# Optimization experiments

Hardware: AMD Instinct MI355X
Metric: run time of the kernel (lower is better)

## Reference

```python
import jax, jax.numpy as jnp
import numpy as np
from jax import lax

STRIDE = (1, 1)
PADDING = ((1, 1), (1, 1))
DILATION = (1, 1)
GROUPS = 1


def setup_inputs() -> dict:
    key = jax.random.key(0)
    k1, k2, k3, k4, k5 = jax.random.split(key, 5)
    # quantized int8-ish activations/weights stored as float (as in the torch module)
    x = jax.random.randint(k1, (32, 128, 56, 56), -128, 128).astype(jnp.float32)
    weight_int = jax.random.randint(k2, (256, 128, 3, 3), -128, 128).astype(jnp.float32)
    bias_int = jax.random.randint(k3, (256,), -1024, 1024).astype(jnp.float32)
    A = jax.random.randint(k4, (256,), 1, 32768)  # per-channel requant multiplier
    N = jax.random.randint(k5, (256,), 16, 25)    # per-channel shift
    return {
        "x": x,
        "weight_int": weight_int,
        "bias_int": bias_int,
        "A": A,
        "N": N,
        "out_min": 0,
        "out_max": 255,
    }


def reference(x, weight_int, bias_int, A, N, out_min, out_max):
    # emulate torch's x.int().float() truncation casts
    xq = jnp.trunc(x)
    wq = jnp.trunc(weight_int)
    bq = jnp.trunc(bias_int)
    out = lax.conv_general_dilated(
        xq, wq,
        window_strides=STRIDE,
        padding=PADDING,
        rhs_dilation=DILATION,
        feature_group_count=GROUPS,
        dimension_numbers=("NCHW", "OIHW", "NCHW"),
    )
    out = jnp.round(out + bq[None, :, None, None])
    # out *= A ; out >>= N  (torch float rshift == divide by 2**N)
    Af = A.astype(jnp.float32)[None, :, None, None]
    Nf = N.astype(jnp.float32)[None, :, None, None]
    out = out * Af / jnp.exp2(Nf)
    if out_min >= 0:
        out = jnp.clip(jnp.round(out), float(out_min), float(out_max))
    return out
```

## Files before the change

### kernel.cpp

```cpp
#include <hip/hip_runtime.h>
#include <stdint.h>

typedef int   v4i __attribute__((ext_vector_type(4)));
typedef float v4f __attribute__((ext_vector_type(4)));

#define XT_H_STRIDE (66*128)
#define XT_N_STRIDE (58*66*128)
#define XT_BYTES    (32*58*66*128)
#define WQ_BYTES    (256*1152)

__device__ __forceinline__ void gload16(const void* g, void* l) {
  __builtin_amdgcn_global_load_lds(
      (const __attribute__((address_space(1))) void*)g,
      (__attribute__((address_space(3))) void*)l, 16, 0, 0);
}

__global__ __launch_bounds__(256) void xform_x(const float* __restrict__ x,
                                               char* __restrict__ xt) {
  __shared__ int LB[56 * 33];
  int bid = blockIdx.x;
  int n  = bid / 58;
  int hp = bid - n * 58;
  int t  = threadIdx.x;
  int srch = hp - 1;
  bool rowok = (srch >= 0) && (srch < 56);
  char* dstrow = xt + (size_t)n * XT_N_STRIDE + (size_t)hp * XT_H_STRIDE;

  if (rowok) {
    const float* rb = x + ((size_t)(n * 128) * 56 + srch) * 56;
#pragma unroll
    for (int u0 = 0; u0 < 2; ++u0) {
      int u  = t + u0 * 256;
      int wb = u & 15;
      int cb = u >> 4;
      int w0 = wb * 4, ci0 = cb * 4;
      if (w0 < 56) {
        int dw[4] = {0, 0, 0, 0};
#pragma unroll
        for (int i = 0; i < 4; ++i) {
          v4f f = *(const v4f*)(rb + (size_t)(ci0 + i) * 3136 + w0);
#pragma unroll
          for (int j = 0; j < 4; ++j)
            dw[j] |= (((int)f[j]) & 255) << (8 * i);
        }
#pragma unroll
        for (int j = 0; j < 4; ++j)
          LB[(w0 + j) * 33 + cb] = dw[j];
      }
    }
    __syncthreads();
    for (int c = t; c < 528; c += 256) {
      int wp  = c >> 3;
      int cio = c & 7;
      int srw = wp - 1;
      v4i v = {0, 0, 0, 0};
      if (srw >= 0 && srw < 56) {
#pragma unroll
        for (int k = 0; k < 4; ++k) v[k] = LB[srw * 33 + cio * 4 + k];
      }
      *(v4i*)(dstrow + c * 16) = v;
    }
  } else {
    v4i z = {0, 0, 0, 0};
    for (int c = t; c < 528; c += 256) *(v4i*)(dstrow + c * 16) = z;
  }
}

__global__ __launch_bounds__(256) void xform_w(const float* __restrict__ wsrc,
                                               const int* __restrict__ Aq,
                                               const int* __restrict__ Nq,
                                               char* __restrict__ wq2,
                                               float* __restrict__ scale) {
  int idx = blockIdx.x * 256 + threadIdx.x;
  int co = idx / 1152;
  int k  = idx - co * 1152;
  int g  = k >> 7;
  int ci = k & 127;
  int kh = g / 3;
  int kw = g - 3 * kh;
  float f = wsrc[(size_t)(co * 128 + ci) * 9 + kh * 3 + kw];
  wq2[((k >> 6) * 256 + co) * 64 + (k & 63)] = (signed char)(int)f;
  if (idx < 256) {
    scale[idx] = (float)Aq[idx] * exp2f(-(float)Nq[idx]);
  }
}

__global__ __launch_bounds__(256, 4) void qconv_gemm(
    const char* __restrict__ xt, const char* __restrict__ wq2,
    const float* __restrict__ bias, const float* __restrict__ scale,
    const int* __restrict__ pmin, const int* __restrict__ pmax,
    float* __restrict__ out) {
  __shared__ __align__(16) char Bp[4 * 8448];

  int bid = blockIdx.x;
  int xcd = bid & 7;
  int q   = bid >> 3;
  int mt  = q & 1;
  int nt  = xcd * 112 + (q >> 1);
  int n   = nt / 28;
  int ht  = nt - n * 28;
  int h0  = ht * 2;
  int m0  = mt * 128;

  int t  = threadIdx.x;
  int wv = t >> 6;
  int ln = t & 63;
  int quad = ln >> 4;
  int l16  = ln & 15;
  int wm = wv & 1, wn = wv >> 1;

  const char* xb = xt + (size_t)n * XT_N_STRIDE + (size_t)h0 * XT_H_STRIDE;

  for (int it = 0; it < 9; ++it) {
    int s = t + it * 256;
    if (s < 2112) {
      int row = s / 528;
      int rr  = s - row * 528;
      int w   = rr >> 3;
      int cq  = rr & 7;
      gload16(xb + row * XT_H_STRIDE + w * 128 + ((cq ^ (w & 7)) << 4),
              Bp + it * 4096 + wv * 1024);
    }
  }
  asm volatile("s_waitcnt vmcnt(0)" ::: "memory");
  asm volatile("s_barrier" ::: "memory");

  v4i acc[4][4];
#pragma unroll
  for (int i = 0; i < 4; ++i)
#pragma unroll
    for (int j = 0; j < 4; ++j) {
      v4i z = {0, 0, 0, 0};
      acc[i][j] = z;
    }

  const char* abase = wq2 + (size_t)(m0 + wm * 64 + l16) * 64 + quad * 16;

  for (int kt = 0; kt < 18; ++kt) {
    int p  = kt & 1;
    int g  = kt >> 1;
    int kh = g / 3;
    int kw = g - 3 * kh;

    v4i a[4], b[4];
    const char* akt = abase + ((size_t)kt << 14);
#pragma unroll
    for (int i = 0; i < 4; ++i)
      a[i] = *(const v4i*)(akt + i * 1024);

    int bswz = (((p << 2) + quad) ^ ((l16 + kw) & 7)) << 4;
    const char* bbase = Bp + (wn + kh) * XT_H_STRIDE + (l16 + kw) * 128 + bswz;
#pragma unroll
    for (int j = 0; j < 4; ++j)
      b[j] = *(const v4i*)(bbase + j * 2048);

#pragma unroll
    for (int i = 0; i < 4; ++i)
#pragma unroll
      for (int j = 0; j < 4; ++j)
        acc[i][j] = __builtin_amdgcn_mfma_i32_16x16x64_i8(a[i], b[j], acc[i][j], 0, 0, 0);
  }

  float mn = (float)pmin[0];
  float mx = (float)pmax[0];
#pragma unroll
  for (int i = 0; i < 4; ++i) {
    int co_b = m0 + wm * 64 + i * 16 + quad * 4;
#pragma unroll
    for (int r = 0; r < 4; ++r) {
      int co = co_b + r;
      float bs = bias[co];
      float sc = scale[co];
#pragma unroll
      for (int j = 0; j < 4; ++j) {
        int sl = wn * 64 + j * 16 + l16;
        int w  = sl & 63;
        int dh = sl >> 6;
        if (w < 56) {
          float f = (float)acc[i][j][r] + bs;
          f = rintf(f * sc);
          f = fminf(fmaxf(f, mn), mx);
          out[(((size_t)n * 256 + co) * 56 + (h0 + dh)) * 56 + w] = f;
        }
      }
    }
  }
}

extern "C" void kernel_launch(void* const* d_in, const int* in_sizes, int n_in,
                              void* d_out, int out_size, void* d_ws, size_t ws_size,
                              hipStream_t stream) {
  const float* x  = (const float*)d_in[0];
  const float* w  = (const float*)d_in[1];
  const float* b  = (const float*)d_in[2];
  const int*   Aq = (const int*)d_in[3];
  const int*   Nq = (const int*)d_in[4];
  const int*   mn = (const int*)d_in[5];
  const int*   mx = (const int*)d_in[6];
  float* out = (float*)d_out;

  char*  xt    = (char*)d_ws;
  char*  wq2   = xt + XT_BYTES;
  float* scale = (float*)(wq2 + WQ_BYTES);

  hipLaunchKernelGGL(xform_x, dim3(32 * 58), dim3(256), 0, stream, x, xt);
  hipLaunchKernelGGL(xform_w, dim3(1152), dim3(256), 0, stream, w, Aq, Nq, wq2, scale);
  hipLaunchKernelGGL(qconv_gemm, dim3(1792), dim3(256), 0, stream,
                     xt, wq2, b, scale, mn, mx, out);
}
```

Measured before the change: 194.3 us.

## Prefetch weight fragments three k-steps ahead with per-wave staggered k order

Keeps a three-deep register ring of A (weight) fragments, issuing their global loads before the LDS fill and three iterations ahead inside the fully unrolled k loop, so MFMAs no longer wait on global loads. Each wave starts its k sequence at a different offset to spread weight-load and LDS bank traffic. Output stores become nontemporal, and the launch-bounds occupancy hint drops from 4 to 3 blocks per CU to make room for the extra registers. The cost is higher register pressure and lower occupancy.

Measured after the change: 210.8 us. +8.5%, slower.

```diff
diff --git a/kernel.cpp b/kernel.cpp
--- a/kernel.cpp
+++ b/kernel.cpp
@@ -85,7 +85,7 @@
   }
 }
 
-__global__ __launch_bounds__(256, 4) void qconv_gemm(
+__global__ __launch_bounds__(256, 3) void qconv_gemm(
     const char* __restrict__ xt, const char* __restrict__ wq2,
     const float* __restrict__ bias, const float* __restrict__ scale,
     const int* __restrict__ pmin, const int* __restrict__ pmax,
@@ -111,6 +111,20 @@
 
   const char* xb = xt + (size_t)n * XT_N_STRIDE + (size_t)h0 * XT_H_STRIDE;
 
+  const char* abase = wq2 + (size_t)(m0 + wm * 64 + l16) * 64 + quad * 16;
+
+  int c5 = wv * 5;
+
+  v4i areg[3][4];
+#pragma unroll
+  for (int d = 0; d < 3; ++d) {
+    int kt = d + c5; if (kt >= 18) kt -= 18;
+    const char* akt = abase + ((size_t)kt << 14);
+#pragma unroll
+    for (int i = 0; i < 4; ++i)
+      areg[d][i] = *(const v4i*)(akt + i * 1024);
+  }
+
   for (int it = 0; it < 9; ++it) {
     int s = t + it * 256;
     if (s < 2112) {
@@ -134,22 +148,17 @@
       acc[i][j] = z;
     }
 
-  const char* abase = wq2 + (size_t)(m0 + wm * 64 + l16) * 64 + quad * 16;
-
-  for (int kt = 0; kt < 18; ++kt) {
-    int p  = kt & 1;
+#pragma unroll
+  for (int uu = 0; uu < 18; ++uu) {
+    int slot = uu % 3;
+    int kt = uu + c5; if (kt >= 18) kt -= 18;
     int g  = kt >> 1;
     int kh = g / 3;
     int kw = g - 3 * kh;
 
-    v4i a[4], b[4];
-    const char* akt = abase + ((size_t)kt << 14);
-#pragma unroll
-    for (int i = 0; i < 4; ++i)
-      a[i] = *(const v4i*)(akt + i * 1024);
-
-    int bswz = (((p << 2) + quad) ^ ((l16 + kw) & 7)) << 4;
+    int bswz = ((((kt & 1) << 2) + quad) ^ ((l16 + kw) & 7)) << 4;
     const char* bbase = Bp + (wn + kh) * XT_H_STRIDE + (l16 + kw) * 128 + bswz;
+    v4i b[4];
 #pragma unroll
     for (int j = 0; j < 4; ++j)
       b[j] = *(const v4i*)(bbase + j * 2048);
@@ -158,7 +167,15 @@
     for (int i = 0; i < 4; ++i)
 #pragma unroll
       for (int j = 0; j < 4; ++j)
-        acc[i][j] = __builtin_amdgcn_mfma_i32_16x16x64_i8(a[i], b[j], acc[i][j], 0, 0, 0);
+        acc[i][j] = __builtin_amdgcn_mfma_i32_16x16x64_i8(areg[slot][i], b[j], acc[i][j], 0, 0, 0);
+
+    if (uu + 3 < 18) {
+      int kt3 = uu + 3 + c5; if (kt3 >= 18) kt3 -= 18;
+      const char* akt = abase + ((size_t)kt3 << 14);
+#pragma unroll
+      for (int i = 0; i < 4; ++i)
+        areg[slot][i] = *(const v4i*)(akt + i * 1024);
+    }
   }
 
   float mn = (float)pmin[0];
@@ -171,16 +188,16 @@
       int co = co_b + r;
       float bs = bias[co];
       float sc = scale[co];
+      float* orow = out + (((size_t)n * 256 + co) * 56 + (h0 + wn)) * 56;
 #pragma unroll
       for (int j = 0; j < 4; ++j) {
         int sl = wn * 64 + j * 16 + l16;
         int w  = sl & 63;
-        int dh = sl >> 6;
         if (w < 56) {
           float f = (float)acc[i][j][r] + bs;
           f = rintf(f * sc);
           f = fminf(fmaxf(f, mn), mx);
-          out[(((size_t)n * 256 + co) * 56 + (h0 + dh)) * 56 + w] = f;
+          __builtin_nontemporal_store(f, orow + w);
         }
       }
     }
```
